# Kernel tuning notes

Measured on AMD Instinct MI355X. Metric: run time of the kernel, lower is better.

## Reference

```python
import jax, jax.numpy as jnp
import numpy as np

B, S, IN, H, NT, NC = 64, 512, 300, 512, 9, 2


def _lstm_dir(x, mask, Wih, Whh, bih, bhh):
    # x: [B,S,IN], mask: [B,S] bool. Packed-sequence semantics: state frozen and
    # output zeroed at padded steps (matches pack_padded/pad_packed).
    xw = jnp.einsum('bsd,gd->bsg', x, Wih) + bih + bhh  # [B,S,4H]

    def step(carry, inp):
        h, c = carry
        xw_t, m = inp
        gates = xw_t + h @ Whh.T
        i, f, g, o = jnp.split(gates, 4, axis=-1)  # torch gate order i,f,g,o
        c_new = jax.nn.sigmoid(f) * c + jax.nn.sigmoid(i) * jnp.tanh(g)
        h_new = jax.nn.sigmoid(o) * jnp.tanh(c_new)
        m1 = m[:, None]
        return (jnp.where(m1, h_new, h), jnp.where(m1, c_new, c)), jnp.where(m1, h_new, 0.0)

    h0 = jnp.zeros((x.shape[0], Whh.shape[1]), x.dtype)
    _, outs = jax.lax.scan(step, (h0, h0), (xw.transpose(1, 0, 2), mask.T))
    return outs.transpose(1, 0, 2)  # [B,S,H]


def _crf_llh(em, tags, mask, start, end, trans):
    # torchcrf log-likelihood, batch_first. em [B,L,T], tags [B,L], mask [B,L] bool.
    Bn = em.shape[0]
    score0 = start[tags[:, 0]] + em[jnp.arange(Bn), 0, tags[:, 0]]

    def num_step(s, inp):
        em_t, tp, tc, m = inp
        e = jnp.take_along_axis(em_t, tc[:, None], 1)[:, 0]
        return s + (trans[tp, tc] + e) * m, None

    num, _ = jax.lax.scan(num_step, score0, (em[:, 1:].transpose(1, 0, 2), tags[:, :-1].T, tags[:, 1:].T, mask[:, 1:].T.astype(em.dtype)))
    last_idx = mask.sum(1).astype(jnp.int32) - 1
    last_tag = jnp.take_along_axis(tags, last_idx[:, None], 1)[:, 0]
    num = num + end[last_tag]

    alpha0 = start[None, :] + em[:, 0]

    def den_step(a, inp):
        em_t, m = inp
        nxt = jax.nn.logsumexp(a[:, :, None] + trans[None] + em_t[:, None, :], axis=1)
        return jnp.where(m[:, None], nxt, a), None

    alpha, _ = jax.lax.scan(den_step, alpha0, (em[:, 1:].transpose(1, 0, 2), mask[:, 1:].T))
    den = jax.nn.logsumexp(alpha + end[None, :], axis=1)
    return num - den


def _crf_decode(em, mask, start, end, trans):
    # Viterbi with identity backpointers at masked steps (= per-seq-end backtrack).
    Bn, L, Tn = em.shape
    score0 = start[None, :] + em[:, 0]
    ident = jnp.broadcast_to(jnp.arange(Tn), (Bn, Tn))

    def step(s, inp):
        em_t, m = inp
        cand = s[:, :, None] + trans[None]  # [B,T_prev,T_next]
        nxt = jnp.max(cand, axis=1) + em_t
        hist = jnp.where(m[:, None], jnp.argmax(cand, axis=1), ident)
        return jnp.where(m[:, None], nxt, s), hist

    score, hist = jax.lax.scan(step, score0, (em[:, 1:].transpose(1, 0, 2), mask[:, 1:].T))
    last_tag = jnp.argmax(score + end[None, :], axis=1)

    def back(tag, h):
        return jnp.take_along_axis(h, tag[:, None], 1)[:, 0], tag

    first_tag, tags_rest = jax.lax.scan(back, last_tag, hist, reverse=True)
    tags = jnp.concatenate([first_tag[None], tags_rest], axis=0).T  # [B,L]
    return jnp.where(mask, tags, -1)


def setup_inputs():
    key = jax.random.key(0)
    ks = jax.random.split(key, 23)
    lengths = jax.random.randint(ks[0], (B,), S // 2, S + 1)
    attention_mask = (jnp.arange(S)[None, :] < lengths[:, None]).astype(jnp.int32)
    input_ids = jax.random.normal(ks[1], (B, S, IN), jnp.float32)
    base = jax.random.randint(ks[2], (B, S), 0, NT)
    drop = jax.random.uniform(ks[3], (B, S)) < 0.15
    drop = drop.at[:, 0].set(False)  # guarantee mask[:,0] all True for CRF
    token_labels = jnp.where((attention_mask == 1) & (~drop), base, -100).astype(jnp.int32)
    seq_labels = jax.random.randint(ks[4], (B,), 0, NC)
    seq_class_weight = jax.random.uniform(ks[5], (NC,), jnp.float32, 0.5, 1.5)
    k = 1.0 / np.sqrt(H)
    u = lambda kk, shape: jax.random.uniform(kk, shape, jnp.float32, -k, k)
    return {
        'input_ids': input_ids, 'attention_mask': attention_mask,
        'seq_labels': seq_labels, 'token_labels': token_labels,
        'seq_class_weight': seq_class_weight,
        'Wih_f': u(ks[6], (4 * H, IN)), 'Whh_f': u(ks[7], (4 * H, H)),
        'bih_f': u(ks[8], (4 * H,)), 'bhh_f': u(ks[9], (4 * H,)),
        'Wih_r': u(ks[10], (4 * H, IN)), 'Whh_r': u(ks[11], (4 * H, H)),
        'bih_r': u(ks[12], (4 * H,)), 'bhh_r': u(ks[13], (4 * H,)),
        'Wtok': u(ks[14], (NT, 2 * H)), 'btok': u(ks[15], (NT,)),
        'Wd': u(ks[16], (2 * H, 2 * H)), 'bd': u(ks[17], (2 * H,)),
        'Wo': u(ks[18], (NC, 2 * H)), 'bo': u(ks[19], (NC,)),
        'crf_start': 0.1 * jax.random.normal(ks[20], (NT,)),
        'crf_end': 0.1 * jax.random.normal(ks[21], (NT,)),
        'crf_trans': 0.1 * jax.random.normal(ks[22], (NT, NT)),
    }


def reference(input_ids, attention_mask, seq_labels, token_labels, seq_class_weight,
              Wih_f, Whh_f, bih_f, bhh_f, Wih_r, Whh_r, bih_r, bhh_r,
              Wtok, btok, Wd, bd, Wo, bo, crf_start, crf_end, crf_trans):
    mask = attention_mask.astype(bool)
    lengths = attention_mask.sum(1).astype(jnp.int32)
    # BiLSTM with packed-sequence semantics
    out_f = _lstm_dir(input_ids, mask, Wih_f, Whh_f, bih_f, bhh_f)
    rev_idx = jnp.clip(lengths[:, None] - 1 - jnp.arange(S)[None, :], 0, S - 1)
    x_rev = jnp.take_along_axis(input_ids, rev_idx[:, :, None], 1)
    out_r_rev = _lstm_dir(x_rev, mask, Wih_r, Whh_r, bih_r, bhh_r)
    out_r = jnp.take_along_axis(out_r_rev, rev_idx[:, :, None], 1) * mask[:, :, None]
    output = jnp.concatenate([out_f, out_r], axis=-1)  # [B,S,2H]
    out_forward = jnp.take_along_axis(out_f, (lengths - 1)[:, None, None], 1)[:, 0]
    out_reverse = out_r[:, 0]
    out_reduced = jnp.concatenate([out_forward, out_reverse], axis=1)  # [B,2H]
    token_logits = output @ Wtok.T + btok  # [B,S,NT]
    seq_logits = jnp.tanh(out_reduced @ Wd.T + bd) @ Wo.T + bo  # [B,NC]
    # ragged re-pack: labelled tokens to front per row (pad_sequence equivalent)
    valid = token_labels >= 0
    order = jnp.argsort(jnp.logical_not(valid), axis=1)  # stable sort
    new_logits = jnp.take_along_axis(token_logits, order[:, :, None], 1)
    new_labels = jnp.take_along_axis(token_labels, order, 1)
    new_mask = new_labels >= 0
    active = jnp.where(new_mask, new_labels, 0)
    llh = _crf_llh(new_logits, active, new_mask, crf_start, crf_end, crf_trans)
    crf_loss = -(llh.sum() / new_mask.sum())  # reduction='token_mean', then -mean
    tags = _crf_decode(new_logits, new_mask, crf_start, crf_end, crf_trans)
    # weighted CE for sequence head
    logp = jax.nn.log_softmax(seq_logits, axis=-1)
    w = seq_class_weight[seq_labels]
    seq_loss = -(w * jnp.take_along_axis(logp, seq_labels[:, None], 1)[:, 0]).sum() / w.sum()
    loss = 1.0 * crf_loss + seq_loss  # token_lambda = 1
    return loss, token_logits, seq_logits, tags
```

## Files before the change

### kernel.cpp

```cpp
#include <hip/hip_runtime.h>
#include <math.h>


struct StepParams {
  const float* x;
  const float* Wih_f; const float* Whh_f; const float* bih_f; const float* bhh_f;
  const float* Wih_r; const float* Whh_r; const float* bih_r; const float* bhh_r;
  const float* h_src; float* h_dst; float* c_buf; float* outcat; float* h_red;
  const int* lengths; int t;
};

__global__ void __launch_bounds__(64) prep_kernel(const int* amask, const int* tok_labels,
                                                  int* lengths, int* nv_arr, int* vidx,
                                                  float* accums, float* state0) {
  int b = blockIdx.x, lane = threadIdx.x;
  int s = 0;
  for (int i = lane; i < 512; i += 64) s += amask[b * 512 + i];
  for (int off = 32; off; off >>= 1) s += __shfl_down(s, off);
  if (lane == 0) lengths[b] = s;
  if (b == 0 && lane < 8) accums[lane] = 0.f;
  for (int i = b * 64 + lane; i < 196608; i += 64 * 64) state0[i] = 0.f;
  if (lane == 0) {
    int nv = 0;
    for (int p = 0; p < 512; ++p) {
      if (tok_labels[b * 512 + p] >= 0) vidx[b * 512 + (nv++)] = p;
    }
    nv_arr[b] = nv;
  }
}

#define FMA4(hv, w0, w1, w2, w3)                                   \
  a0 += hv.x*w0.x + hv.y*w0.y + hv.z*w0.z + hv.w*w0.w;             \
  a1 += hv.x*w1.x + hv.y*w1.y + hv.z*w1.z + hv.w*w1.w;             \
  a2 += hv.x*w2.x + hv.y*w2.y + hv.z*w2.z + hv.w*w2.w;             \
  a3 += hv.x*w3.x + hv.y*w3.y + hv.z*w3.z + hv.w*w3.w;

__global__ void __launch_bounds__(256) lstm_step(StepParams P) {
  const int wg  = blockIdx.x;
  const int dir = wg & 1;
  const int jg  = wg >> 1;
  const int tid = threadIdx.x;
  const int b    = tid & 63;
  const int slot = tid >> 6;
  const int j  = (jg << 2) + slot;
  const int t  = P.t;

  const float* Wih = dir ? P.Wih_r : P.Wih_f;
  const float* Whh = dir ? P.Whh_r : P.Whh_f;
  const float* bih = dir ? P.bih_r : P.bih_f;
  const float* bhh = dir ? P.bhh_r : P.bhh_f;

  __shared__ float buf[64][132];
  __shared__ int len_sh[64];
  if (tid < 64) len_sh[tid] = P.lengths[tid];

  float a0 = bih[j]        + bhh[j];
  float a1 = bih[512 + j]  + bhh[512 + j];
  float a2 = bih[1024 + j] + bhh[1024 + j];
  float a3 = bih[1536 + j] + bhh[1536 + j];

  const int len = P.lengths[b];
  const size_t sidx = (size_t)(dir * 64 + b) * 512 + j;
  const float c_old = P.c_buf[sidx];
  const float h_old = P.h_src[sidx];

  for (int cidx = 0; cidx < 2; ++cidx) {
    const int kc = cidx << 7;
    __syncthreads();
    for (int i4 = tid; i4 < 2048; i4 += 256) {
      int bb = i4 >> 5;
      int kq = (i4 & 31) << 2;
      int pos;
      if (dir) { pos = len_sh[bb] - 1 - t; if (pos < 0) pos = 0; }
      else pos = t;
      float4 v = *(const float4*)(P.x + ((size_t)bb * 512 + pos) * 300 + kc + kq);
      *(float4*)&buf[bb][kq] = v;
    }
    __syncthreads();
    const float* wr0 = Wih + (size_t)(j)        * 300 + kc;
    const float* wr1 = Wih + (size_t)(512 + j)  * 300 + kc;
    const float* wr2 = Wih + (size_t)(1024 + j) * 300 + kc;
    const float* wr3 = Wih + (size_t)(1536 + j) * 300 + kc;
    for (int k = 0; k < 128; k += 4) {
      float4 hv = *(const float4*)&buf[b][k];
      float4 w0 = *(const float4*)(wr0 + k);
      float4 w1 = *(const float4*)(wr1 + k);
      float4 w2 = *(const float4*)(wr2 + k);
      float4 w3 = *(const float4*)(wr3 + k);
      FMA4(hv, w0, w1, w2, w3)
    }
  }
  {
    const int kc = 256;
    __syncthreads();
    for (int i4 = tid; i4 < 704; i4 += 256) {
      int bb = i4 / 11;
      int kq = (i4 - bb * 11) << 2;
      int pos;
      if (dir) { pos = len_sh[bb] - 1 - t; if (pos < 0) pos = 0; }
      else pos = t;
      float4 v = *(const float4*)(P.x + ((size_t)bb * 512 + pos) * 300 + kc + kq);
      *(float4*)&buf[bb][kq] = v;
    }
    __syncthreads();
    const float* wr0 = Wih + (size_t)(j)        * 300 + kc;
    const float* wr1 = Wih + (size_t)(512 + j)  * 300 + kc;
    const float* wr2 = Wih + (size_t)(1024 + j) * 300 + kc;
    const float* wr3 = Wih + (size_t)(1536 + j) * 300 + kc;
    for (int k = 0; k < 44; k += 4) {
      float4 hv = *(const float4*)&buf[b][k];
      float4 w0 = *(const float4*)(wr0 + k);
      float4 w1 = *(const float4*)(wr1 + k);
      float4 w2 = *(const float4*)(wr2 + k);
      float4 w3 = *(const float4*)(wr3 + k);
      FMA4(hv, w0, w1, w2, w3)
    }
  }

  for (int cidx = 0; cidx < 4; ++cidx) {
    const int kc = cidx << 7;
    __syncthreads();
    for (int i4 = tid; i4 < 2048; i4 += 256) {
      int bb = i4 >> 5;
      int kq = (i4 & 31) << 2;
      float4 v = *(const float4*)(P.h_src + (size_t)(dir * 64 + bb) * 512 + kc + kq);
      *(float4*)&buf[bb][kq] = v;
    }
    __syncthreads();
    const float* wr0 = Whh + (size_t)(j)        * 512 + kc;
    const float* wr1 = Whh + (size_t)(512 + j)  * 512 + kc;
    const float* wr2 = Whh + (size_t)(1024 + j) * 512 + kc;
    const float* wr3 = Whh + (size_t)(1536 + j) * 512 + kc;
    for (int k = 0; k < 128; k += 4) {
      float4 hv = *(const float4*)&buf[b][k];
      float4 w0 = *(const float4*)(wr0 + k);
      float4 w1 = *(const float4*)(wr1 + k);
      float4 w2 = *(const float4*)(wr2 + k);
      float4 w3 = *(const float4*)(wr3 + k);
      FMA4(hv, w0, w1, w2, w3)
    }
  }

  const bool act = (t < len);
  float ig = 1.f / (1.f + expf(-a0));
  float fg = 1.f / (1.f + expf(-a1));
  float gg = tanhf(a2);
  float og = 1.f / (1.f + expf(-a3));
  float cn = fg * c_old + ig * gg;
  float hn = og * tanhf(cn);
  const float c_st = act ? cn : c_old;
  const float h_st = act ? hn : h_old;
  P.c_buf[sidx] = c_st;
  P.h_dst[sidx] = h_st;

  if (dir == 0) {
    P.outcat[((size_t)b * 512 + t) * 1024 + j] = act ? hn : 0.f;
  } else {
    if (act) P.outcat[((size_t)b * 512 + (len - 1 - t)) * 1024 + 512 + j] = hn;
    int sc = len + t;
    if (sc < 512) P.outcat[((size_t)b * 512 + sc) * 1024 + 512 + j] = 0.f;
  }
  if (t == len - 1) P.h_red[(size_t)b * 1024 + dir * 512 + j] = hn;
}

__global__ void __launch_bounds__(256) tok_kernel(const float* outcat, const float* Wtok,
                                                  const float* btok, float* out_tok) {
  __shared__ float wt[9 * 1024];
  __shared__ float bt[9];
  for (int i = threadIdx.x; i < 9216; i += 256) wt[i] = Wtok[i];
  if (threadIdx.x < 9) bt[threadIdx.x] = btok[threadIdx.x];
  __syncthreads();
  int wave = threadIdx.x >> 6, lane = threadIdx.x & 63;
  for (int r0 = 0; r0 < 32; ++r0) {
    int row = blockIdx.x * 128 + wave * 32 + r0;
    const float* src = outcat + (size_t)row * 1024;
    float f[16];
#pragma unroll
    for (int q = 0; q < 16; ++q) f[q] = src[lane + 64 * q];
#pragma unroll
    for (int n = 0; n < 9; ++n) {
      float s = 0.f;
#pragma unroll
      for (int q = 0; q < 16; ++q) s += f[q] * wt[n * 1024 + lane + 64 * q];
      for (int off = 32; off; off >>= 1) s += __shfl_down(s, off);
      if (lane == 0) out_tok[(size_t)row * 9 + n] = s + bt[n];
    }
  }
}

__global__ void __launch_bounds__(256) seq_kernel(const float* h_red, const float* Wd,
                                                  const float* bd, const float* Wo,
                                                  const float* bo, const float* scw,
                                                  const int* seq_labels, float* out_seq,
                                                  float* accums) {
  int bidx = blockIdx.x;
  __shared__ float xs[1024];
  __shared__ float ds[1024];
  __shared__ float red[8];
  for (int i = threadIdx.x; i < 1024; i += 256) xs[i] = h_red[(size_t)bidx * 1024 + i];
  __syncthreads();
  int wave = threadIdx.x >> 6, lane = threadIdx.x & 63;
  for (int oi = 0; oi < 256; ++oi) {
    int o = wave * 256 + oi;
    const float* wrow = Wd + (size_t)o * 1024;
    float s = 0.f;
#pragma unroll
    for (int q = 0; q < 16; ++q) s += xs[lane + 64 * q] * wrow[lane + 64 * q];
    for (int off = 32; off; off >>= 1) s += __shfl_down(s, off);
    if (lane == 0) ds[o] = tanhf(s + bd[o]);
  }
  __syncthreads();
  float p0 = 0.f, p1 = 0.f;
  for (int i = threadIdx.x; i < 1024; i += 256) {
    float dv = ds[i];
    p0 += dv * Wo[i];
    p1 += dv * Wo[1024 + i];
  }
  for (int off = 32; off; off >>= 1) { p0 += __shfl_down(p0, off); p1 += __shfl_down(p1, off); }
  if (lane == 0) { red[wave] = p0; red[4 + wave] = p1; }
  __syncthreads();
  if (threadIdx.x == 0) {
    float l0 = red[0] + red[1] + red[2] + red[3] + bo[0];
    float l1 = red[4] + red[5] + red[6] + red[7] + bo[1];
    out_seq[bidx * 2 + 0] = l0;
    out_seq[bidx * 2 + 1] = l1;
    float m = fmaxf(l0, l1);
    float lse = m + logf(expf(l0 - m) + expf(l1 - m));
    int lbl = seq_labels[bidx];
    float w = scw[lbl];
    float logp = (lbl ? l1 : l0) - lse;
    atomicAdd(&accums[2], -w * logp);
    atomicAdd(&accums[3], w);
  }
}

__global__ void __launch_bounds__(64) crf_kernel(const float* tok_logits, const int* tok_labels,
                                                 const int* vidx, const int* nv_arr,
                                                 const float* startv, const float* endv,
                                                 const float* trans, float* tags_out,
                                                 float* accums) {
  int b = blockIdx.x, lane = threadIdx.x;
  __shared__ int vsh[512];
  __shared__ int lsh[512];
  __shared__ unsigned char hist[512][16];
  __shared__ int tag_sh[512];
  const int nv = nv_arr[b];
  for (int p = lane; p < 512; p += 64) {
    int v = (p < nv) ? vidx[b * 512 + p] : 0;
    vsh[p] = v;
    lsh[p] = tok_labels[b * 512 + v];
  }
  __syncthreads();

  const int n = lane;
  const bool activeN = (n < 9);
  const int nc = activeN ? n : 0;
  float tcol[9];
#pragma unroll
  for (int mm = 0; mm < 9; ++mm) tcol[mm] = trans[mm * 9 + nc];

  const float* emb = tok_logits + (size_t)b * 512 * 9;
  float em0 = emb[(size_t)vsh[0] * 9 + nc];
  float alpha = startv[nc] + em0;
  if (!activeN) alpha = -1e30f;
  float vsc = alpha;
  int labprev = lsh[0];
  float num = __shfl(alpha, labprev);

  for (int p = 1; p < 512; ++p) {
    const bool m_p = (p < nv);
    float emn = m_p ? emb[(size_t)vsh[p] * 9 + nc] : 0.f;
    float mx = -1e30f, best = -1e30f;
    int arg = 0;
    float cand[9];
#pragma unroll
    for (int mm = 0; mm < 9; ++mm) {
      float am = __shfl(alpha, mm);
      float vm = __shfl(vsc, mm);
      float cm = am + tcol[mm];
      float vc = vm + tcol[mm];
      cand[mm] = cm;
      mx = fmaxf(mx, cm);
      if (vc > best) { best = vc; arg = mm; }
    }
    float s = 0.f;
#pragma unroll
    for (int mm = 0; mm < 9; ++mm) s += expf(cand[mm] - mx);
    float nxt = mx + logf(s) + emn;
    float nsc = best + emn;
    int h = n;
    if (m_p) {
      h = arg;
      if (activeN) { alpha = nxt; vsc = nsc; }
    }
    if (activeN) hist[p][n] = (unsigned char)h;
    if (m_p) {
      int lab = lsh[p];
      float e_lab = __shfl(emn, lab);
      num += trans[labprev * 9 + lab] + e_lab;
      labprev = lab;
    }
  }
  num += endv[labprev];

  float aend = activeN ? (alpha + endv[nc]) : -1e30f;
  float vend = activeN ? (vsc + endv[nc]) : -1e30f;
  float mx2 = -1e30f, best2 = -1e30f;
  int ltag = 0;
#pragma unroll
  for (int mm = 0; mm < 9; ++mm) {
    float am = __shfl(aend, mm);
    float vm = __shfl(vend, mm);
    mx2 = fmaxf(mx2, am);
    if (vm > best2) { best2 = vm; ltag = mm; }
  }
  float s2 = 0.f;
#pragma unroll
  for (int mm = 0; mm < 9; ++mm) { float am = __shfl(aend, mm); s2 += expf(am - mx2); }
  float den = mx2 + logf(s2);

  if (lane == 0) {
    atomicAdd(&accums[0], num - den);
    atomicAdd(&accums[1], (float)nv);
    int tg = ltag;
    for (int p = 511; p >= 1; --p) { tag_sh[p] = tg; tg = hist[p][tg]; }
    tag_sh[0] = tg;
  }
  __syncthreads();
  for (int p = lane; p < 512; p += 64)
    tags_out[(size_t)b * 512 + p] = (p < nv) ? (float)tag_sh[p] : -1.0f;
}

__global__ void loss_kernel(const float* accums, float* out_loss) {
  if (threadIdx.x == 0 && blockIdx.x == 0)
    out_loss[0] = -(accums[0] / accums[1]) + accums[2] / accums[3];
}

extern "C" void kernel_launch(void* const* d_in, const int* in_sizes, int n_in,
                              void* d_out, int out_size, void* d_ws, size_t ws_size,
                              hipStream_t stream) {
  const float* x          = (const float*)d_in[0];
  const int*   amask      = (const int*)d_in[1];
  const int*   seq_labels = (const int*)d_in[2];
  const int*   tok_labels = (const int*)d_in[3];
  const float* scw        = (const float*)d_in[4];
  const float* Wih_f = (const float*)d_in[5];
  const float* Whh_f = (const float*)d_in[6];
  const float* bih_f = (const float*)d_in[7];
  const float* bhh_f = (const float*)d_in[8];
  const float* Wih_r = (const float*)d_in[9];
  const float* Whh_r = (const float*)d_in[10];
  const float* bih_r = (const float*)d_in[11];
  const float* bhh_r = (const float*)d_in[12];
  const float* Wtok  = (const float*)d_in[13];
  const float* btok  = (const float*)d_in[14];
  const float* Wd    = (const float*)d_in[15];
  const float* bd    = (const float*)d_in[16];
  const float* Wo    = (const float*)d_in[17];
  const float* bo    = (const float*)d_in[18];
  const float* crf_start = (const float*)d_in[19];
  const float* crf_end   = (const float*)d_in[20];
  const float* crf_trans = (const float*)d_in[21];

  float* ws = (float*)d_ws;
  float* h_a    = ws;
  float* h_b    = ws + 65536;
  float* c_buf  = ws + 131072;
  float* h_red  = ws + 196608;
  int*   lengths = (int*)(ws + 262144);
  int*   nv_arr  = (int*)(ws + 262208);
  int*   vidx    = (int*)(ws + 262272);
  float* accums  = ws + 295040;
  float* outcat  = ws + 295168;

  float* out      = (float*)d_out;
  float* out_loss = out;
  float* out_tok  = out + 1;
  float* out_seq  = out + 294913;
  float* out_tags = out + 295041;

  prep_kernel<<<64, 64, 0, stream>>>(amask, tok_labels, lengths, nv_arr, vidx, accums, h_a);

  for (int t = 0; t < 512; ++t) {
    StepParams sp;
    sp.x = x;
    sp.Wih_f = Wih_f; sp.Whh_f = Whh_f; sp.bih_f = bih_f; sp.bhh_f = bhh_f;
    sp.Wih_r = Wih_r; sp.Whh_r = Whh_r; sp.bih_r = bih_r; sp.bhh_r = bhh_r;
    sp.h_src = (t & 1) ? h_b : h_a;
    sp.h_dst = (t & 1) ? h_a : h_b;
    sp.c_buf = c_buf; sp.outcat = outcat; sp.h_red = h_red;
    sp.lengths = lengths; sp.t = t;
    lstm_step<<<256, 256, 0, stream>>>(sp);
  }

  tok_kernel<<<256, 256, 0, stream>>>(outcat, Wtok, btok, out_tok);
  seq_kernel<<<64, 256, 0, stream>>>(h_red, Wd, bd, Wo, bo, scw, seq_labels, out_seq, accums);
  crf_kernel<<<64, 64, 0, stream>>>(out_tok, tok_labels, vidx, nv_arr,
                                    crf_start, crf_end, crf_trans, out_tags, accums);
  loss_kernel<<<1, 64, 0, stream>>>(accums, out_loss);
}
```

Before: 503.7 ms.

## Precompute LSTM input projection for all timesteps before recurrent loop

Adds a batched xw_kernel that computes x·Wih^T plus biases for every timestep and both directions into a large workspace buffer. The per-step recurrent kernel then loads this precomputed gate input instead of recomputing the 300-wide input projection inside the serial loop, which shortens the critical path of each of the 512 steps. The cost is a large workspace (about 512MB) and one big upfront kernel. The path is gated on the workspace being large enough, with the old path kept as a fallback.

```diff
diff --git a/kernel.cpp b/kernel.cpp
--- a/kernel.cpp
+++ b/kernel.cpp
@@ -7,6 +7,7 @@
   const float* Wih_f; const float* Whh_f; const float* bih_f; const float* bhh_f;
   const float* Wih_r; const float* Whh_r; const float* bih_r; const float* bhh_r;
   const float* h_src; float* h_dst; float* c_buf; float* outcat; float* h_red;
+  const float* xw;
   const int* lengths; int t;
 };
 
@@ -35,6 +36,90 @@
   a2 += hv.x*w2.x + hv.y*w2.y + hv.z*w2.z + hv.w*w2.w;             \
   a3 += hv.x*w3.x + hv.y*w3.y + hv.z*w3.z + hv.w*w3.w;
 
+__global__ void __launch_bounds__(256) xw_kernel(const float* x,
+                                                 const float* Wih_f, const float* bih_f, const float* bhh_f,
+                                                 const float* Wih_r, const float* bih_r, const float* bhh_r,
+                                                 const int* lengths, float* xw) {
+  const int bid  = blockIdx.x;
+  const int dir  = bid >> 14;
+  const int rem  = bid & 16383;
+  const int t    = rem >> 5;
+  const int jg16 = rem & 31;
+  const int tid  = threadIdx.x;
+  const int b    = tid & 63;
+  const int slot = tid >> 6;
+  const int j0   = jg16 * 16 + slot * 4;
+
+  const float* Wih = dir ? Wih_r : Wih_f;
+  const float* bih = dir ? bih_r : bih_f;
+  const float* bhh = dir ? bhh_r : bhh_f;
+
+  __shared__ float buf[64][132];
+  __shared__ int len_sh[64];
+  if (tid < 64) len_sh[tid] = lengths[tid];
+
+  float acc[4][4];
+#pragma unroll
+  for (int jj = 0; jj < 4; ++jj)
+#pragma unroll
+    for (int g = 0; g < 4; ++g)
+      acc[jj][g] = bih[g * 512 + j0 + jj] + bhh[g * 512 + j0 + jj];
+
+  for (int cidx = 0; cidx < 3; ++cidx) {
+    const int kc   = cidx << 7;
+    const int klen = (cidx == 2) ? 44 : 128;
+    __syncthreads();
+    if (cidx < 2) {
+      for (int i4 = tid; i4 < 2048; i4 += 256) {
+        int bb = i4 >> 5;
+        int kq = (i4 & 31) << 2;
+        int pos;
+        if (dir) { pos = len_sh[bb] - 1 - t; if (pos < 0) pos = 0; }
+        else pos = t;
+        float4 v = *(const float4*)(x + ((size_t)bb * 512 + pos) * 300 + kc + kq);
+        *(float4*)&buf[bb][kq] = v;
+      }
+    } else {
+      for (int i4 = tid; i4 < 704; i4 += 256) {
+        int bb = i4 / 11;
+        int kq = (i4 - bb * 11) << 2;
+        int pos;
+        if (dir) { pos = len_sh[bb] - 1 - t; if (pos < 0) pos = 0; }
+        else pos = t;
+        float4 v = *(const float4*)(x + ((size_t)bb * 512 + pos) * 300 + kc + kq);
+        *(float4*)&buf[bb][kq] = v;
+      }
+    }
+    __syncthreads();
+#pragma unroll
+    for (int jj = 0; jj < 4; ++jj) {
+      const int j = j0 + jj;
+      const float* wr0 = Wih + (size_t)(j)        * 300 + kc;
+      const float* wr1 = Wih + (size_t)(512 + j)  * 300 + kc;
+      const float* wr2 = Wih + (size_t)(1024 + j) * 300 + kc;
+      const float* wr3 = Wih + (size_t)(1536 + j) * 300 + kc;
+      float a0 = acc[jj][0], a1 = acc[jj][1], a2 = acc[jj][2], a3 = acc[jj][3];
+      for (int k = 0; k < klen; k += 4) {
+        float4 hv = *(const float4*)&buf[b][k];
+        float4 w0 = *(const float4*)(wr0 + k);
+        float4 w1 = *(const float4*)(wr1 + k);
+        float4 w2 = *(const float4*)(wr2 + k);
+        float4 w3 = *(const float4*)(wr3 + k);
+        FMA4(hv, w0, w1, w2, w3)
+      }
+      acc[jj][0] = a0; acc[jj][1] = a1; acc[jj][2] = a2; acc[jj][3] = a3;
+    }
+  }
+
+  float* base = xw + ((size_t)(dir * 512 + t) * 2048) * 64 + b;
+#pragma unroll
+  for (int jj = 0; jj < 4; ++jj)
+#pragma unroll
+    for (int g = 0; g < 4; ++g)
+      base[(size_t)(g * 512 + j0 + jj) * 64] = acc[jj][g];
+}
+
+template <bool USE_XW>
 __global__ void __launch_bounds__(256) lstm_step(StepParams P) {
   const int wg  = blockIdx.x;
   const int dir = wg & 1;
@@ -45,75 +130,87 @@
   const int j  = (jg << 2) + slot;
   const int t  = P.t;
 
-  const float* Wih = dir ? P.Wih_r : P.Wih_f;
   const float* Whh = dir ? P.Whh_r : P.Whh_f;
-  const float* bih = dir ? P.bih_r : P.bih_f;
-  const float* bhh = dir ? P.bhh_r : P.bhh_f;
 
   __shared__ float buf[64][132];
   __shared__ int len_sh[64];
   if (tid < 64) len_sh[tid] = P.lengths[tid];
 
-  float a0 = bih[j]        + bhh[j];
-  float a1 = bih[512 + j]  + bhh[512 + j];
-  float a2 = bih[1024 + j] + bhh[1024 + j];
-  float a3 = bih[1536 + j] + bhh[1536 + j];
+  float a0, a1, a2, a3;
+  if constexpr (USE_XW) {
+    const float* xwp = P.xw + ((size_t)(dir * 512 + t) * 2048) * 64 + b;
+    a0 = xwp[(size_t)(j)        * 64];
+    a1 = xwp[(size_t)(512 + j)  * 64];
+    a2 = xwp[(size_t)(1024 + j) * 64];
+    a3 = xwp[(size_t)(1536 + j) * 64];
+  } else {
+    const float* bih = dir ? P.bih_r : P.bih_f;
+    const float* bhh = dir ? P.bhh_r : P.bhh_f;
+    a0 = bih[j]        + bhh[j];
+    a1 = bih[512 + j]  + bhh[512 + j];
+    a2 = bih[1024 + j] + bhh[1024 + j];
+    a3 = bih[1536 + j] + bhh[1536 + j];
+  }
 
   const int len = P.lengths[b];
   const size_t sidx = (size_t)(dir * 64 + b) * 512 + j;
   const float c_old = P.c_buf[sidx];
   const float h_old = P.h_src[sidx];
 
-  for (int cidx = 0; cidx < 2; ++cidx) {
-    const int kc = cidx << 7;
-    __syncthreads();
-    for (int i4 = tid; i4 < 2048; i4 += 256) {
-      int bb = i4 >> 5;
-      int kq = (i4 & 31) << 2;
-      int pos;
-      if (dir) { pos = len_sh[bb] - 1 - t; if (pos < 0) pos = 0; }
-      else pos = t;
-      float4 v = *(const float4*)(P.x + ((size_t)bb * 512 + pos) * 300 + kc + kq);
-      *(float4*)&buf[bb][kq] = v;
-    }
-    __syncthreads();
-    const float* wr0 = Wih + (size_t)(j)        * 300 + kc;
-    const float* wr1 = Wih + (size_t)(512 + j)  * 300 + kc;
-    const float* wr2 = Wih + (size_t)(1024 + j) * 300 + kc;
-    const float* wr3 = Wih + (size_t)(1536 + j) * 300 + kc;
-    for (int k = 0; k < 128; k += 4) {
-      float4 hv = *(const float4*)&buf[b][k];
-      float4 w0 = *(const float4*)(wr0 + k);
-      float4 w1 = *(const float4*)(wr1 + k);
-      float4 w2 = *(const float4*)(wr2 + k);
-      float4 w3 = *(const float4*)(wr3 + k);
-      FMA4(hv, w0, w1, w2, w3)
-    }
-  }
-  {
-    const int kc = 256;
-    __syncthreads();
-    for (int i4 = tid; i4 < 704; i4 += 256) {
-      int bb = i4 / 11;
-      int kq = (i4 - bb * 11) << 2;
-      int pos;
-      if (dir) { pos = len_sh[bb] - 1 - t; if (pos < 0) pos = 0; }
-      else pos = t;
-      float4 v = *(const float4*)(P.x + ((size_t)bb * 512 + pos) * 300 + kc + kq);
-      *(float4*)&buf[bb][kq] = v;
-    }
-    __syncthreads();
-    const float* wr0 = Wih + (size_t)(j)        * 300 + kc;
-    const float* wr1 = Wih + (size_t)(512 + j)  * 300 + kc;
-    const float* wr2 = Wih + (size_t)(1024 + j) * 300 + kc;
-    const float* wr3 = Wih + (size_t)(1536 + j) * 300 + kc;
-    for (int k = 0; k < 44; k += 4) {
-      float4 hv = *(const float4*)&buf[b][k];
-      float4 w0 = *(const float4*)(wr0 + k);
-      float4 w1 = *(const float4*)(wr1 + k);
-      float4 w2 = *(const float4*)(wr2 + k);
-      float4 w3 = *(const float4*)(wr3 + k);
-      FMA4(hv, w0, w1, w2, w3)
+  if constexpr (!USE_XW) {
+    const float* Wih = dir ? P.Wih_r : P.Wih_f;
+    for (int cidx = 0; cidx < 2; ++cidx) {
+      const int kc = cidx << 7;
+      __syncthreads();
+      for (int i4 = tid; i4 < 2048; i4 += 256) {
+        int bb = i4 >> 5;
+        int kq = (i4 & 31) << 2;
+        int pos;
+        if (dir) { pos = len_sh[bb] - 1 - t; if (pos < 0) pos = 0; }
+        else pos = t;
+        float4 v = *(const float4*)(P.x + ((size_t)bb * 512 + pos) * 300 + kc + kq);
+        *(float4*)&buf[bb][kq] = v;
+      }
+      __syncthreads();
+      const float* wr0 = Wih + (size_t)(j)        * 300 + kc;
+      const float* wr1 = Wih + (size_t)(512 + j)  * 300 + kc;
+      const float* wr2 = Wih + (size_t)(1024 + j) * 300 + kc;
+      const float* wr3 = Wih + (size_t)(1536 + j) * 300 + kc;
+      for (int k = 0; k < 128; k += 4) {
+        float4 hv = *(const float4*)&buf[b][k];
+        float4 w0 = *(const float4*)(wr0 + k);
+        float4 w1 = *(const float4*)(wr1 + k);
+        float4 w2 = *(const float4*)(wr2 + k);
+        float4 w3 = *(const float4*)(wr3 + k);
+        FMA4(hv, w0, w1, w2, w3)
+      }
+    }
+    {
+      const int kc = 256;
+      __syncthreads();
+      for (int i4 = tid; i4 < 704; i4 += 256) {
+        int bb = i4 / 11;
+        int kq = (i4 - bb * 11) << 2;
+        int pos;
+        if (dir) { pos = len_sh[bb] - 1 - t; if (pos < 0) pos = 0; }
+        else pos = t;
+        float4 v = *(const float4*)(P.x + ((size_t)bb * 512 + pos) * 300 + kc + kq);
+        *(float4*)&buf[bb][kq] = v;
+      }
+      __syncthreads();
+      const float* Wih2 = Wih;
+      const float* wr0 = Wih2 + (size_t)(j)        * 300 + kc;
+      const float* wr1 = Wih2 + (size_t)(512 + j)  * 300 + kc;
+      const float* wr2 = Wih2 + (size_t)(1024 + j) * 300 + kc;
+      const float* wr3 = Wih2 + (size_t)(1536 + j) * 300 + kc;
+      for (int k = 0; k < 44; k += 4) {
+        float4 hv = *(const float4*)&buf[b][k];
+        float4 w0 = *(const float4*)(wr0 + k);
+        float4 w1 = *(const float4*)(wr1 + k);
+        float4 w2 = *(const float4*)(wr2 + k);
+        float4 w3 = *(const float4*)(wr3 + k);
+        FMA4(hv, w0, w1, w2, w3)
+      }
     }
   }
 
@@ -372,6 +469,9 @@
   int*   vidx    = (int*)(ws + 262272);
   float* accums  = ws + 295040;
   float* outcat  = ws + 295168;
+  float* xw      = ws + 33849600;
+
+  const bool use_xw = (ws_size >= 672269312ull);
 
   float* out      = (float*)d_out;
   float* out_loss = out;
@@ -380,6 +480,11 @@
   float* out_tags = out + 295041;
 
   prep_kernel<<<64, 64, 0, stream>>>(amask, tok_labels, lengths, nv_arr, vidx, accums, h_a);
+
+  if (use_xw) {
+    xw_kernel<<<32768, 256, 0, stream>>>(x, Wih_f, bih_f, bhh_f, Wih_r, bih_r, bhh_r,
+                                         lengths, xw);
+  }
 
   for (int t = 0; t < 512; ++t) {
     StepParams sp;
@@ -389,8 +494,10 @@
     sp.h_src = (t & 1) ? h_b : h_a;
     sp.h_dst = (t & 1) ? h_a : h_b;
     sp.c_buf = c_buf; sp.outcat = outcat; sp.h_red = h_red;
+    sp.xw = xw;
     sp.lengths = lengths; sp.t = t;
-    lstm_step<<<256, 256, 0, stream>>>(sp);
+    if (use_xw) lstm_step<true><<<256, 256, 0, stream>>>(sp);
+    else        lstm_step<false><<<256, 256, 0, stream>>>(sp);
   }
 
   tok_kernel<<<256, 256, 0, stream>>>(outcat, Wtok, btok, out_tok);
```

Result: no change. 502.9 ms (-0.2%).
